# Optimization experiments

Hardware: AMD Instinct MI355X
Metric: run time of the kernel (lower is better)

## Reference

```python
import jax, jax.numpy as jnp
import numpy as np

N = 500_000
D_IN, D_HID, NUM_HEADS, D_OUT = 256, 128, 4, 4


def setup_inputs() -> dict:
    key = jax.random.key(0)
    k1, k2, k3, k4 = jax.random.split(key, 4)
    x = jax.random.normal(k1, (N, D_IN), dtype=jnp.float32)
    W1 = jax.random.normal(k2, (D_IN, D_HID), dtype=jnp.float32)
    W2 = jax.random.normal(k3, (D_HID, D_OUT), dtype=jnp.float32)
    heads = jax.random.randint(k4, (N,), 0, NUM_HEADS, dtype=jnp.int32)
    return {"x": x, "W1": W1, "W2": W2, "heads": heads}


def reference(x, W1, W2, heads):
    # linear_1: e3nn Linear over pure-scalar irreps == dense matmul with
    # path normalization 1/sqrt(fan_in)
    h = (x @ W1) * (1.0 / np.sqrt(D_IN))          # [N, D_HID]
    # gated nonlinearity (scalars only -> plain activation)
    h = jax.nn.silu(h)
    # mask_head: channels grouped into NUM_HEADS blocks of D_HID//NUM_HEADS;
    # keep only the block matching each node's head
    hb = h.reshape(N, NUM_HEADS, D_HID // NUM_HEADS)
    onehot = jax.nn.one_hot(heads, NUM_HEADS, dtype=h.dtype)  # [N, H]
    h = (hb * onehot[:, :, None]).reshape(N, D_HID)
    # linear_2
    return (h @ W2) * (1.0 / np.sqrt(D_HID))      # [N, D_OUT]
```

## Files before the change

### kernel.cpp

```cpp
#include <hip/hip_runtime.h>
#include <hip/hip_bf16.h>


#define D_IN   256
#define D_HID  128
#define TILE_M 64
#define XPAD   264
#define HPAD   36

typedef __attribute__((ext_vector_type(8))) short  short8;
typedef __attribute__((ext_vector_type(4))) float  float4v;

__device__ __forceinline__ unsigned short f2bf_rne(float f) {
    union { float f; unsigned int u; } cv; cv.f = f;
    unsigned int u = cv.u;
    return (unsigned short)((u + 0x7FFFu + ((u >> 16) & 1u)) >> 16);
}

__global__ void prep_w1(const float* __restrict__ W1, unsigned short* __restrict__ W1p) {
    int idx = blockIdx.x * 256 + threadIdx.x;
    int i = idx >> 7;
    int j = idx & 127;
    unsigned short b = f2bf_rne(W1[idx] * 0.0625f);
    int kt = i >> 5, q = (i >> 3) & 3, jj = i & 7;
    int nt = j >> 4, m = j & 15;
    int lane = q * 16 + m;
    W1p[(((kt * 8 + nt) * 64 + lane) << 3) + jj] = b;
}

__global__ __launch_bounds__(256)
void readout_kernel(const float* __restrict__ x,
                    const unsigned short* __restrict__ W1p,
                    const float* __restrict__ W2,
                    const int* __restrict__ heads,
                    float* __restrict__ out, int nrows) {
    __shared__ unsigned short xs[TILE_M * XPAD];
    __shared__ float hk[TILE_M * HPAD];
    __shared__ int hs[TILE_M];

    const int t    = threadIdx.x;
    const int row0 = blockIdx.x * TILE_M;

    if (t < TILE_M) {
        int gr = row0 + t;
        hs[t] = (gr < nrows) ? heads[gr] : 0;
    }

    #pragma unroll
    for (int it = 0; it < 16; ++it) {
        int idx = it * 256 + t;
        int r   = idx >> 6;
        int cg  = idx & 63;
        float4v v = {0.f, 0.f, 0.f, 0.f};
        int gr = row0 + r;
        if (gr < nrows) v = *(const float4v*)(x + (size_t)gr * D_IN + cg * 4);
        ushort4 b;
        b.x = f2bf_rne(v[0]); b.y = f2bf_rne(v[1]);
        b.z = f2bf_rne(v[2]); b.w = f2bf_rne(v[3]);
        *(ushort4*)(&xs[r * XPAD + cg * 4]) = b;
    }
    __syncthreads();

    const int lane = t & 63;
    const int w    = t >> 6;
    const int q    = lane >> 4;
    const int m    = lane & 15;

    float4v acc[4][2];
    #pragma unroll
    for (int rt = 0; rt < 4; ++rt)
        #pragma unroll
        for (int c = 0; c < 2; ++c) acc[rt][c] = (float4v){0.f, 0.f, 0.f, 0.f};

    #pragma unroll
    for (int kt = 0; kt < 8; ++kt) {
        short8 a[4], b[2];
        #pragma unroll
        for (int rt = 0; rt < 4; ++rt) {
            const unsigned short* p = &xs[(rt * 16 + m) * XPAD + kt * 32 + q * 8];
            a[rt] = *(const short8*)p;
        }
        #pragma unroll
        for (int c = 0; c < 2; ++c) {
            int nt = 2 * w + c;
            b[c] = *(const short8*)(W1p + (((kt * 8 + nt) * 64 + lane) << 3));
        }
        #pragma unroll
        for (int rt = 0; rt < 4; ++rt)
            #pragma unroll
            for (int c = 0; c < 2; ++c)
                acc[rt][c] = __builtin_amdgcn_mfma_f32_16x16x32_bf16(a[rt], b[c], acc[rt][c], 0, 0, 0);
    }

    #pragma unroll
    for (int rt = 0; rt < 4; ++rt)
        #pragma unroll
        for (int c = 0; c < 2; ++c)
            #pragma unroll
            for (int reg = 0; reg < 4; ++reg) {
                int row = rt * 16 + q * 4 + reg;
                if (hs[row] == w)
                    hk[row * HPAD + c * 16 + m] = acc[rt][c][reg];
            }
    __syncthreads();

    {
        int row  = t >> 2;
        int c8   = (t & 3) * 8;
        int head = hs[row];
        float4v o = {0.f, 0.f, 0.f, 0.f};
        float4v h0 = *(const float4v*)(&hk[row * HPAD + c8]);
        float4v h1 = *(const float4v*)(&hk[row * HPAD + c8 + 4]);
        #pragma unroll
        for (int jj = 0; jj < 8; ++jj) {
            float h = (jj < 4) ? h0[jj] : h1[jj - 4];
            float s = h / (1.0f + __expf(-h));
            int gj = head * 32 + c8 + jj;
            float4v w2 = *(const float4v*)(W2 + gj * 4);
            o += w2 * s;
        }
        #pragma unroll
        for (int d = 1; d < 4; d <<= 1) {
            #pragma unroll
            for (int e = 0; e < 4; ++e) o[e] += __shfl_xor(o[e], d, 64);
        }
        if ((t & 3) == 0) {
            int gr = row0 + row;
            if (gr < nrows) {
                const float sc = 0.08838834764831845f;
                float4v res = { o[0] * sc, o[1] * sc, o[2] * sc, o[3] * sc };
                *(float4v*)(out + (size_t)gr * 4) = res;
            }
        }
    }
}

extern "C" void kernel_launch(void* const* d_in, const int* in_sizes, int n_in,
                              void* d_out, int out_size, void* d_ws, size_t ws_size,
                              hipStream_t stream) {
    const float* x     = (const float*)d_in[0];
    const float* W1    = (const float*)d_in[1];
    const float* W2    = (const float*)d_in[2];
    const int*   heads = (const int*)d_in[3];
    float*       out   = (float*)d_out;
    unsigned short* W1p = (unsigned short*)d_ws;

    int nrows = in_sizes[0] / D_IN;

    prep_w1<<<128, 256, 0, stream>>>(W1, W1p);
    int nb = (nrows + TILE_M - 1) / TILE_M;
    readout_kernel<<<nb, 256, 0, stream>>>(x, W1p, W2, heads, out, nrows);
}
```

Before: 727.5 us.

## Load x straight into MFMA registers, drop LDS staging and per-wave head split

Each wave now owns 32 rows and computes all 128 hidden columns itself. The A operand is loaded directly from global memory into registers and converted to bf16 there, instead of being staged through LDS. The head-masked SiLU and the second linear layer run in registers with a 16-lane shuffle reduction, which removes the LDS buffers and both __syncthreads. The cost is that all 64 KB of W1p is read per wave from cache, and the x loads are strided per lane (32-byte chunks per row), which may coalesce worse than the old row-contiguous float4 loads. The change also computes all four heads' columns and then selects one.

Result: faster. 709.1 us (-2.5%).

```diff
diff --git a/kernel.cpp b/kernel.cpp
--- a/kernel.cpp
+++ b/kernel.cpp
@@ -3,18 +3,25 @@
 
 
 #define D_IN   256
-#define D_HID  128
-#define TILE_M 64
-#define XPAD   264
-#define HPAD   36
+#define TILE_M 128
 
 typedef __attribute__((ext_vector_type(8))) short  short8;
 typedef __attribute__((ext_vector_type(4))) float  float4v;
+typedef __attribute__((ext_vector_type(4))) int    int4v;
 
 __device__ __forceinline__ unsigned short f2bf_rne(float f) {
     union { float f; unsigned int u; } cv; cv.f = f;
     unsigned int u = cv.u;
     return (unsigned short)((u + 0x7FFFu + ((u >> 16) & 1u)) >> 16);
+}
+
+__device__ __forceinline__ short8 pack8(float4v lo, float4v hi) {
+    short8 r;
+    r[0] = (short)f2bf_rne(lo[0]); r[1] = (short)f2bf_rne(lo[1]);
+    r[2] = (short)f2bf_rne(lo[2]); r[3] = (short)f2bf_rne(lo[3]);
+    r[4] = (short)f2bf_rne(hi[0]); r[5] = (short)f2bf_rne(hi[1]);
+    r[6] = (short)f2bf_rne(hi[2]); r[7] = (short)f2bf_rne(hi[3]);
+    return r;
 }
 
 __global__ void prep_w1(const float* __restrict__ W1, unsigned short* __restrict__ W1p) {
@@ -23,113 +30,92 @@
     int j = idx & 127;
     unsigned short b = f2bf_rne(W1[idx] * 0.0625f);
     int kt = i >> 5, q = (i >> 3) & 3, jj = i & 7;
-    int nt = j >> 4, m = j & 15;
-    int lane = q * 16 + m;
+    int nt = j >> 4, mm = j & 15;
+    int lane = q * 16 + mm;
     W1p[(((kt * 8 + nt) * 64 + lane) << 3) + jj] = b;
 }
 
 __global__ __launch_bounds__(256)
-void readout_kernel(const float* __restrict__ x,
-                    const unsigned short* __restrict__ W1p,
-                    const float* __restrict__ W2,
-                    const int* __restrict__ heads,
-                    float* __restrict__ out, int nrows) {
-    __shared__ unsigned short xs[TILE_M * XPAD];
-    __shared__ float hk[TILE_M * HPAD];
-    __shared__ int hs[TILE_M];
-
+void readout_v2(const float* __restrict__ x,
+                const unsigned short* __restrict__ W1p,
+                const float* __restrict__ W2,
+                const int* __restrict__ heads,
+                float* __restrict__ out, int nrows) {
     const int t    = threadIdx.x;
-    const int row0 = blockIdx.x * TILE_M;
-
-    if (t < TILE_M) {
-        int gr = row0 + t;
-        hs[t] = (gr < nrows) ? heads[gr] : 0;
-    }
-
-    #pragma unroll
-    for (int it = 0; it < 16; ++it) {
-        int idx = it * 256 + t;
-        int r   = idx >> 6;
-        int cg  = idx & 63;
-        float4v v = {0.f, 0.f, 0.f, 0.f};
-        int gr = row0 + r;
-        if (gr < nrows) v = *(const float4v*)(x + (size_t)gr * D_IN + cg * 4);
-        ushort4 b;
-        b.x = f2bf_rne(v[0]); b.y = f2bf_rne(v[1]);
-        b.z = f2bf_rne(v[2]); b.w = f2bf_rne(v[3]);
-        *(ushort4*)(&xs[r * XPAD + cg * 4]) = b;
-    }
-    __syncthreads();
-
+    const int w    = t >> 6;
     const int lane = t & 63;
-    const int w    = t >> 6;
     const int q    = lane >> 4;
     const int m    = lane & 15;
+    const int rowbase = blockIdx.x * TILE_M + w * 32;
 
-    float4v acc[4][2];
+    const int r0 = min(rowbase + m,      nrows - 1);
+    const int r1 = min(rowbase + 16 + m, nrows - 1);
+    const float* xr0 = x + (size_t)r0 * D_IN + q * 8;
+    const float* xr1 = x + (size_t)r1 * D_IN + q * 8;
+    const unsigned short* bbase = W1p + lane * 8;
+
+    float4v acc[2][8];
     #pragma unroll
-    for (int rt = 0; rt < 4; ++rt)
+    for (int rt = 0; rt < 2; ++rt)
         #pragma unroll
-        for (int c = 0; c < 2; ++c) acc[rt][c] = (float4v){0.f, 0.f, 0.f, 0.f};
+        for (int nt = 0; nt < 8; ++nt) acc[rt][nt] = (float4v){0.f, 0.f, 0.f, 0.f};
 
     #pragma unroll
     for (int kt = 0; kt < 8; ++kt) {
-        short8 a[4], b[2];
+        float4v a0lo = *(const float4v*)(xr0 + kt * 32);
+        float4v a0hi = *(const float4v*)(xr0 + kt * 32 + 4);
+        float4v a1lo = *(const float4v*)(xr1 + kt * 32);
+        float4v a1hi = *(const float4v*)(xr1 + kt * 32 + 4);
+        short8 b[8];
         #pragma unroll
-        for (int rt = 0; rt < 4; ++rt) {
-            const unsigned short* p = &xs[(rt * 16 + m) * XPAD + kt * 32 + q * 8];
-            a[rt] = *(const short8*)p;
+        for (int nt = 0; nt < 8; ++nt)
+            b[nt] = *(const short8*)(bbase + (kt * 8 + nt) * 512);
+        short8 a0 = pack8(a0lo, a0hi);
+        short8 a1 = pack8(a1lo, a1hi);
+        #pragma unroll
+        for (int nt = 0; nt < 8; ++nt) {
+            acc[0][nt] = __builtin_amdgcn_mfma_f32_16x16x32_bf16(a0, b[nt], acc[0][nt], 0, 0, 0);
+            acc[1][nt] = __builtin_amdgcn_mfma_f32_16x16x32_bf16(a1, b[nt], acc[1][nt], 0, 0, 0);
+        }
+    }
+
+    const float sc = 0.08838834764831845f;
+    const bool full = (rowbase + 32) <= nrows;
+    #pragma unroll
+    for (int rt = 0; rt < 2; ++rt) {
+        int4v hv;
+        if (full) {
+            hv = *(const int4v*)(heads + rowbase + rt * 16 + q * 4);
+        } else {
+            #pragma unroll
+            for (int e = 0; e < 4; ++e)
+                hv[e] = heads[min(rowbase + rt * 16 + q * 4 + e, nrows - 1)];
         }
         #pragma unroll
-        for (int c = 0; c < 2; ++c) {
-            int nt = 2 * w + c;
-            b[c] = *(const short8*)(W1p + (((kt * 8 + nt) * 64 + lane) << 3));
-        }
-        #pragma unroll
-        for (int rt = 0; rt < 4; ++rt)
+        for (int reg = 0; reg < 4; ++reg) {
+            int h = hv[reg];
+            float v0 = (h == 0) ? acc[rt][0][reg] : (h == 1) ? acc[rt][2][reg]
+                     : (h == 2) ? acc[rt][4][reg] : acc[rt][6][reg];
+            float v1 = (h == 0) ? acc[rt][1][reg] : (h == 1) ? acc[rt][3][reg]
+                     : (h == 2) ? acc[rt][5][reg] : acc[rt][7][reg];
+            float s0 = v0 / (1.0f + __expf(-v0));
+            float s1 = v1 / (1.0f + __expf(-v1));
+            float4v w2a = *(const float4v*)(W2 + (h * 32 + m) * 4);
+            float4v w2b = *(const float4v*)(W2 + (h * 32 + 16 + m) * 4);
+            float4v o = w2a * s0 + w2b * s1;
             #pragma unroll
-            for (int c = 0; c < 2; ++c)
-                acc[rt][c] = __builtin_amdgcn_mfma_f32_16x16x32_bf16(a[rt], b[c], acc[rt][c], 0, 0, 0);
-    }
-
-    #pragma unroll
-    for (int rt = 0; rt < 4; ++rt)
-        #pragma unroll
-        for (int c = 0; c < 2; ++c)
-            #pragma unroll
-            for (int reg = 0; reg < 4; ++reg) {
-                int row = rt * 16 + q * 4 + reg;
-                if (hs[row] == w)
-                    hk[row * HPAD + c * 16 + m] = acc[rt][c][reg];
+            for (int d = 1; d < 16; d <<= 1) {
+                o[0] += __shfl_xor(o[0], d, 64);
+                o[1] += __shfl_xor(o[1], d, 64);
+                o[2] += __shfl_xor(o[2], d, 64);
+                o[3] += __shfl_xor(o[3], d, 64);
             }
-    __syncthreads();
-
-    {
-        int row  = t >> 2;
-        int c8   = (t & 3) * 8;
-        int head = hs[row];
-        float4v o = {0.f, 0.f, 0.f, 0.f};
-        float4v h0 = *(const float4v*)(&hk[row * HPAD + c8]);
-        float4v h1 = *(const float4v*)(&hk[row * HPAD + c8 + 4]);
-        #pragma unroll
-        for (int jj = 0; jj < 8; ++jj) {
-            float h = (jj < 4) ? h0[jj] : h1[jj - 4];
-            float s = h / (1.0f + __expf(-h));
-            int gj = head * 32 + c8 + jj;
-            float4v w2 = *(const float4v*)(W2 + gj * 4);
-            o += w2 * s;
-        }
-        #pragma unroll
-        for (int d = 1; d < 4; d <<= 1) {
-            #pragma unroll
-            for (int e = 0; e < 4; ++e) o[e] += __shfl_xor(o[e], d, 64);
-        }
-        if ((t & 3) == 0) {
-            int gr = row0 + row;
-            if (gr < nrows) {
-                const float sc = 0.08838834764831845f;
-                float4v res = { o[0] * sc, o[1] * sc, o[2] * sc, o[3] * sc };
-                *(float4v*)(out + (size_t)gr * 4) = res;
+            if (m == 0) {
+                int gr = rowbase + rt * 16 + q * 4 + reg;
+                if (gr < nrows) {
+                    float4v res = { o[0] * sc, o[1] * sc, o[2] * sc, o[3] * sc };
+                    *(float4v*)(out + (size_t)gr * 4) = res;
+                }
             }
         }
     }
@@ -149,5 +135,5 @@
 
     prep_w1<<<128, 256, 0, stream>>>(W1, W1p);
     int nb = (nrows + TILE_M - 1) / TILE_M;
-    readout_kernel<<<nb, 256, 0, stream>>>(x, W1p, W2, heads, out, nrows);
+    readout_v2<<<nb, 256, 0, stream>>>(x, W1p, W2, heads, out, nrows);
 }
```
